# Optimization experiments

Measured on AMD Instinct MI355X. Metric: run time of the kernel, lower is better.

Reference implementation:

```python
import jax, jax.numpy as jnp
import numpy as np

B, S, H, NH = 2, 2048, 1024, 16
DH = H // NH
FF = 4 * H
EPS = 1e-5


def setup_inputs() -> dict:
    key = jax.random.key(0)
    ks = jax.random.split(key, 16)
    sd = 0.02
    inp = {
        "x": jax.random.normal(ks[0], (B, S, H), dtype=jnp.float32),
        "Wq": jax.random.normal(ks[1], (H, H), dtype=jnp.float32) * sd,
        "bq": jnp.zeros((H,), jnp.float32),
        "Wk": jax.random.normal(ks[2], (H, H), dtype=jnp.float32) * sd,
        "bk": jnp.zeros((H,), jnp.float32),
        "Wv": jax.random.normal(ks[3], (H, H), dtype=jnp.float32) * sd,
        "bv": jnp.zeros((H,), jnp.float32),
        "Wo": jax.random.normal(ks[4], (H, H), dtype=jnp.float32) * sd,
        "bo": jnp.zeros((H,), jnp.float32),
        "W1": jax.random.normal(ks[5], (H, FF), dtype=jnp.float32) * sd,
        "b1": jnp.zeros((FF,), jnp.float32),
        "W2": jax.random.normal(ks[6], (FF, H), dtype=jnp.float32) * sd,
        "b2": jnp.zeros((H,), jnp.float32),
        "g1": jnp.ones((H,), jnp.float32),
        "be1": jnp.zeros((H,), jnp.float32),
        "g2": jnp.ones((H,), jnp.float32),
        "be2": jnp.zeros((H,), jnp.float32),
    }
    return inp


def _layernorm(x, g, b):
    mu = jnp.mean(x, axis=-1, keepdims=True)
    var = jnp.mean(jnp.square(x - mu), axis=-1, keepdims=True)
    return (x - mu) * jax.lax.rsqrt(var + EPS) * g + b


def _block(x, Wq, bq, Wk, bk, Wv, bv, Wo, bo, W1, b1, W2, b2, g1, be1, g2, be2):
    # pre-LN attention
    h = _layernorm(x, g1, be1)
    q = (h @ Wq + bq).reshape(B, S, NH, DH)
    k = (h @ Wk + bk).reshape(B, S, NH, DH)
    v = (h @ Wv + bv).reshape(B, S, NH, DH)
    scale = DH ** -0.5
    scores = jnp.einsum("bqhd,bkhd->bhqk", q, k) * scale  # [B,NH,S,S]
    causal = jnp.tril(jnp.ones((S, S), dtype=bool))
    scores = jnp.where(causal, scores, -jnp.inf)
    attn = jax.nn.softmax(scores, axis=-1)
    out = jnp.einsum("bhqk,bkhd->bqhd", attn, v).reshape(B, S, H)
    x = x + (out @ Wo + bo)
    # pre-LN FFN with exact GELU (torch nn.GELU default)
    h = _layernorm(x, g2, be2)
    h = jax.nn.gelu(h @ W1 + b1, approximate=False)
    return x + (h @ W2 + b2)


def reference(x, Wq, bq, Wk, bk, Wv, bv, Wo, bo, W1, b1, W2, b2, g1, be1, g2, be2):
    return _block(x, Wq, bq, Wk, bk, Wv, bv, Wo, bo, W1, b1, W2, b2, g1, be1, g2, be2)
```

## Files before the change

### kernel.cpp

```cpp
#include <hip/hip_runtime.h>
#include <cstdint>
#include <cstddef>

typedef unsigned short u16;
typedef __attribute__((ext_vector_type(8))) __bf16 bf16v8;
typedef __attribute__((ext_vector_type(8))) unsigned short u16x8;
typedef __attribute__((ext_vector_type(4))) float f32x4;

constexpr int Bc = 2, Sc = 2048, Hc = 1024, NHc = 16, DHc = 64, FFc = 4096;
constexpr int Mc = Bc * Sc;

__device__ __forceinline__ u16 f2bf(float f) {
  unsigned u = __builtin_bit_cast(unsigned, f);
  return (u16)((u + 0x7FFFu + ((u >> 16) & 1u)) >> 16);
}

__device__ __forceinline__ int xcd_swz(int bid, int n) {
  const int q = n >> 3;
  return (bid & 7) * q + (bid >> 3);
}

__device__ __forceinline__ void gload_lds16(const void* g, void* l) {
  __builtin_amdgcn_global_load_lds(
      (const __attribute__((address_space(1))) unsigned*)(uintptr_t)g,
      (__attribute__((address_space(3))) unsigned*)(unsigned)(uintptr_t)l,
      16, 0, 0);
}

__global__ __launch_bounds__(256) void wconv_kernel(const float* __restrict__ W,
                                                    u16* __restrict__ Wt, int K, int N) {
  __shared__ float tile[64][65];
  const int n0 = blockIdx.x << 6, k0 = blockIdx.y << 6;
  const int t = threadIdx.x;
  const int col = t & 63, r0 = t >> 6;
#pragma unroll
  for (int i = 0; i < 16; ++i) {
    int r = (i << 2) + r0;
    tile[r][col] = W[(size_t)(k0 + r) * N + n0 + col];
  }
  __syncthreads();
#pragma unroll
  for (int i = 0; i < 16; ++i) {
    int n = (i << 2) + r0;
    Wt[(size_t)(n0 + n) * K + k0 + col] = f2bf(tile[col][n]);
  }
}

__global__ __launch_bounds__(256) void ln_kernel(const float* __restrict__ x,
                                                 const float* __restrict__ g,
                                                 const float* __restrict__ be,
                                                 u16* __restrict__ y) {
  const int row = blockIdx.x;
  const int t = threadIdx.x;
  const float4 v = ((const float4*)(x + (size_t)row * Hc))[t];
  float s1 = v.x + v.y + v.z + v.w;
  float s2 = v.x * v.x + v.y * v.y + v.z * v.z + v.w * v.w;
#pragma unroll
  for (int o = 32; o > 0; o >>= 1) {
    s1 += __shfl_xor(s1, o);
    s2 += __shfl_xor(s2, o);
  }
  __shared__ float r1[4], r2[4];
  const int wave = t >> 6, lane = t & 63;
  if (lane == 0) { r1[wave] = s1; r2[wave] = s2; }
  __syncthreads();
  s1 = r1[0] + r1[1] + r1[2] + r1[3];
  s2 = r2[0] + r2[1] + r2[2] + r2[3];
  const float mu = s1 * (1.f / Hc);
  const float var = s2 * (1.f / Hc) - mu * mu;
  const float rs = rsqrtf(var + 1e-5f);
  const float4 gv = ((const float4*)g)[t];
  const float4 bv = ((const float4*)be)[t];
  ushort4 ov;
  ov.x = f2bf((v.x - mu) * rs * gv.x + bv.x);
  ov.y = f2bf((v.y - mu) * rs * gv.y + bv.y);
  ov.z = f2bf((v.z - mu) * rs * gv.z + bv.z);
  ov.w = f2bf((v.w - mu) * rs * gv.w + bv.w);
  ((ushort4*)(y + (size_t)row * Hc))[t] = ov;
}

template <int EPI>
__global__ __launch_bounds__(256, 2) void gemm_kernel(
    const u16* __restrict__ A, const u16* __restrict__ Bt,
    const float* __restrict__ bias, const float* __restrict__ res,
    u16* __restrict__ outb, float* __restrict__ outf, float* __restrict__ outf2,
    int N, int Kext, int lda, int ldb, int koff, int nx) {
  __shared__ __align__(16) char smraw[32768];
  u16 (*As)[128][32] = (u16(*)[128][32])smraw;
  u16 (*Bs)[128][32] = (u16(*)[128][32])(smraw + 16384);
  float (*Cs)[16][132] = (float(*)[16][132])smraw;

  const int t = threadIdx.x;
  const int wave = t >> 6, lane = t & 63;
  const int pid = xcd_swz(blockIdx.x, gridDim.x);
  const int bn = pid % nx, bm = pid / nx;
  const int kz = blockIdx.z;
  A += (size_t)kz * koff;
  Bt += (size_t)kz * koff;
  const int wm = wave >> 1, wn = wave & 1;
  const int fr = lane & 15, fk = (lane >> 4) << 3;

  f32x4 acc[4][4] = {};

  const int srow = (wave << 4) + (lane >> 2);
  const int scol = (lane & 3) << 3;
  const u16* Ag0 = A + (size_t)(bm * 128 + srow) * lda + scol;
  const u16* Ag1 = Ag0 + (size_t)64 * lda;
  const u16* Bg0 = Bt + (size_t)(bn * 128 + srow) * ldb + scol;
  const u16* Bg1 = Bg0 + (size_t)64 * ldb;

  const int nk = Kext >> 5;
  auto STAGE = [&](int buf, int k0) {
    gload_lds16(Ag0 + k0, &As[buf][wave << 4][0]);
    gload_lds16(Ag1 + k0, &As[buf][64 + (wave << 4)][0]);
    gload_lds16(Bg0 + k0, &Bs[buf][wave << 4][0]);
    gload_lds16(Bg1 + k0, &Bs[buf][64 + (wave << 4)][0]);
  };

  STAGE(0, 0);
  asm volatile("s_waitcnt vmcnt(0)" ::: "memory");
  __syncthreads();
  int cur = 0;
  for (int kt = 0; kt < nk; ++kt) {
    if (kt + 1 < nk) STAGE(cur ^ 1, (kt + 1) << 5);
    bf16v8 af[4], bfr[4];
#pragma unroll
    for (int i = 0; i < 4; ++i) af[i] = *(const bf16v8*)&As[cur][(wm << 6) + (i << 4) + fr][fk];
#pragma unroll
    for (int j = 0; j < 4; ++j) bfr[j] = *(const bf16v8*)&Bs[cur][(wn << 6) + (j << 4) + fr][fk];
    __builtin_amdgcn_s_setprio(1);
#pragma unroll
    for (int i = 0; i < 4; ++i)
#pragma unroll
      for (int j = 0; j < 4; ++j)
        acc[i][j] = __builtin_amdgcn_mfma_f32_16x16x32_bf16(af[i], bfr[j], acc[i][j], 0, 0, 0);
    __builtin_amdgcn_s_setprio(0);
    asm volatile("s_waitcnt vmcnt(0)" ::: "memory");
    __syncthreads();
    cur ^= 1;
  }

  const int cr = (lane >> 4) << 2, cc = lane & 15;
  const int b2 = t >> 7, u = t & 127, lr = u >> 3, c0 = (u & 7) << 4;
  float* fdst = (EPI == 3 && kz) ? outf2 : outf;

  for (int i = 0; i < 4; ++i) {
#pragma unroll
    for (int j = 0; j < 4; ++j) {
      int col = (wn << 6) + (j << 4) + cc;
      float bz = 0.f;
      if constexpr (EPI != 3) bz = bias[(bn << 7) + col];
#pragma unroll
      for (int r = 0; r < 4; ++r) Cs[wm][cr + r][col] = acc[i][j][r] + bz;
    }
    __syncthreads();
    {
      const float* crow = &Cs[b2][lr][c0];
      f32x4 v0 = *(const f32x4*)(crow);
      f32x4 v1 = *(const f32x4*)(crow + 4);
      f32x4 v2 = *(const f32x4*)(crow + 8);
      f32x4 v3 = *(const f32x4*)(crow + 12);
      const int grow = (bm << 7) + (b2 << 6) + (i << 4) + lr;
      const int gc = (bn << 7) + c0;
      const size_t base = (size_t)grow * N + gc;
      if constexpr (EPI == 0 || EPI == 1) {
        float vv[16];
#pragma unroll
        for (int k = 0; k < 4; ++k) { vv[k] = v0[k]; vv[4 + k] = v1[k]; vv[8 + k] = v2[k]; vv[12 + k] = v3[k]; }
        if constexpr (EPI == 1) {
#pragma unroll
          for (int k = 0; k < 16; ++k)
            vv[k] = 0.5f * vv[k] * (1.0f + erff(vv[k] * 0.70710678118654752f));
        }
        u16x8 o0, o1;
#pragma unroll
        for (int k = 0; k < 8; ++k) { o0[k] = f2bf(vv[k]); o1[k] = f2bf(vv[8 + k]); }
        *(u16x8*)&outb[base] = o0;
        *(u16x8*)&outb[base + 8] = o1;
      } else {
        if constexpr (EPI == 2) {
          const f32x4* rp = (const f32x4*)&res[base];
          v0 += rp[0]; v1 += rp[1]; v2 += rp[2]; v3 += rp[3];
        }
        f32x4* op = (f32x4*)&fdst[base];
        op[0] = v0; op[1] = v1; op[2] = v2; op[3] = v3;
      }
    }
    __syncthreads();
  }
}

__global__ __launch_bounds__(256, 2) void qkv_gemm_kernel(
    const u16* __restrict__ A, const u16* __restrict__ Bt,
    const float* __restrict__ bq, const float* __restrict__ bk,
    const float* __restrict__ bv,
    u16* __restrict__ Qb, u16* __restrict__ Kb, u16* __restrict__ Vtg) {
  constexpr int K = 1024;
  __shared__ __align__(16) char smraw[32768];
  u16 (*As)[128][32] = (u16(*)[128][32])smraw;
  u16 (*Bs)[128][32] = (u16(*)[128][32])(smraw + 16384);
  float (*Cs)[16][132] = (float(*)[16][132])smraw;

  const int t = threadIdx.x;
  const int wave = t >> 6, lane = t & 63;
  const int pid = xcd_swz(blockIdx.x, 768);
  const int bn = pid % 24, bm = pid / 24;
  const int wm = wave >> 1, wn = wave & 1;
  const int fr = lane & 15, fk = (lane >> 4) << 3;
  const int seg = bn >> 3;

  f32x4 acc[4][4] = {};

  const int srow = (wave << 4) + (lane >> 2);
  const int scol = (lane & 3) << 3;
  const u16* Ag0 = A + (size_t)(bm * 128 + srow) * K + scol;
  const u16* Ag1 = Ag0 + (size_t)64 * K;
  const u16* Bg0 = Bt + (size_t)(bn * 128 + srow) * K + scol;
  const u16* Bg1 = Bg0 + (size_t)64 * K;

  const int nk = K >> 5;
  auto STAGE = [&](int buf, int k0) {
    gload_lds16(Ag0 + k0, &As[buf][wave << 4][0]);
    gload_lds16(Ag1 + k0, &As[buf][64 + (wave << 4)][0]);
    gload_lds16(Bg0 + k0, &Bs[buf][wave << 4][0]);
    gload_lds16(Bg1 + k0, &Bs[buf][64 + (wave << 4)][0]);
  };

  STAGE(0, 0);
  asm volatile("s_waitcnt vmcnt(0)" ::: "memory");
  __syncthreads();
  int cur = 0;
  for (int kt = 0; kt < nk; ++kt) {
    if (kt + 1 < nk) STAGE(cur ^ 1, (kt + 1) << 5);
    bf16v8 af[4], bfr[4];
#pragma unroll
    for (int i = 0; i < 4; ++i) af[i] = *(const bf16v8*)&As[cur][(wm << 6) + (i << 4) + fr][fk];
#pragma unroll
    for (int j = 0; j < 4; ++j) bfr[j] = *(const bf16v8*)&Bs[cur][(wn << 6) + (j << 4) + fr][fk];
    __builtin_amdgcn_s_setprio(1);
#pragma unroll
    for (int i = 0; i < 4; ++i)
#pragma unroll
      for (int j = 0; j < 4; ++j)
        acc[i][j] = __builtin_amdgcn_mfma_f32_16x16x32_bf16(af[i], bfr[j], acc[i][j], 0, 0, 0);
    __builtin_amdgcn_s_setprio(0);
    asm volatile("s_waitcnt vmcnt(0)" ::: "memory");
    __syncthreads();
    cur ^= 1;
  }

  const int cr = (lane >> 4) << 2, cc = lane & 15;
  const int b2 = t >> 7, u = t & 127, lr = u >> 3, c0 = (u & 7) << 4;
  const float* bp = (seg == 0) ? bq : (seg == 1) ? bk : bv;

  for (int i = 0; i < 4; ++i) {
#pragma unroll
    for (int j = 0; j < 4; ++j) {
      int col = (wn << 6) + (j << 4) + cc;
      float bz = bp[((bn << 7) + col) & 1023];
#pragma unroll
      for (int r = 0; r < 4; ++r) Cs[wm][cr + r][col] = acc[i][j][r] + bz;
    }
    __syncthreads();
    if (seg < 2) {
      const float* crow = &Cs[b2][lr][c0];
      f32x4 v0 = *(const f32x4*)(crow);
      f32x4 v1 = *(const f32x4*)(crow + 4);
      f32x4 v2 = *(const f32x4*)(crow + 8);
      f32x4 v3 = *(const f32x4*)(crow + 12);
      const int grow = (bm << 7) + (b2 << 6) + (i << 4) + lr;
      const int cn0 = (((bn & 7) << 7) + c0);
      u16* dst = (seg == 0) ? Qb : Kb;
      u16x8 o0, o1;
#pragma unroll
      for (int k = 0; k < 4; ++k) {
        o0[k] = f2bf(v0[k]); o0[4 + k] = f2bf(v1[k]);
        o1[k] = f2bf(v2[k]); o1[4 + k] = f2bf(v3[k]);
      }
      *(u16x8*)&dst[(size_t)grow * 1024 + cn0] = o0;
      *(u16x8*)&dst[(size_t)grow * 1024 + cn0 + 8] = o1;
    } else {
      const int cv = ((bn & 7) << 7) + u;
      const int h = cv >> 6, dh = cv & 63;
#pragma unroll
      for (int oct = 0; oct < 2; ++oct) {
        u16x8 o;
#pragma unroll
        for (int k = 0; k < 8; ++k) o[k] = f2bf(Cs[b2][(oct << 3) + k][u]);
        const int srow2 = (bm << 7) + (b2 << 6) + (i << 4) + (oct << 3);
        const int bb = srow2 >> 11, s = srow2 & 2047;
        size_t idx = ((size_t)(bb * 16 + h)) * (64 * 2048) + (size_t)dh * 2048 + s;
        *(u16x8*)&Vtg[idx] = o;
      }
    }
    __syncthreads();
  }
}

__global__ __launch_bounds__(256) void combine_kernel(float* __restrict__ out,
                                                      const float* __restrict__ p0,
                                                      const float* __restrict__ p1,
                                                      const float* __restrict__ bias) {
  const int i = blockIdx.x * 256 + threadIdx.x;
  f32x4 o = ((f32x4*)out)[i];
  f32x4 a = ((const f32x4*)p0)[i];
  f32x4 b = ((const f32x4*)p1)[i];
  const int col = (i << 2) & 1023;
  f32x4 bb = *(const f32x4*)&bias[col];
  o += a + b + bb;
  ((f32x4*)out)[i] = o;
}

__global__ __launch_bounds__(256, 3) void attn_kernel(const u16* __restrict__ Q,
                                                      const u16* __restrict__ Kb,
                                                      const u16* __restrict__ Vt,
                                                      u16* __restrict__ O) {
  constexpr float CS = 0.18033688011112042f;
  constexpr float M2 = 8.0f;
  const int pid = xcd_swz(blockIdx.x, 512);
  const int bx = pid & 15, bh = pid >> 4;
  const int t = threadIdx.x, wave = t >> 6, lane = t & 63;
  const int fr = lane & 15, fk = (lane >> 4) << 3;

  __shared__ u16 Ks[2][64][72];
  __shared__ u16 Vs[2][64][72];
  __shared__ u16 Ps[4][16][72];

  const size_t base = ((size_t)(bh >> 4) * Sc) * Hc + (bh & 15) * DHc;
  const u16* Qp = Q + base;
  const u16* Kp = Kb + base;
  const u16* Vp = Vt + (size_t)bh * (64 * 2048);

  const int r_st = t >> 3;
  const int co_st = (t & 7) << 3;

  bf16v8 ones;
#pragma unroll
  for (int k = 0; k < 8; ++k) ones[k] = (__bf16)1.0f;

  for (int half = 0; half < 2; ++half) {
    const int qt = half ? (31 - bx) : bx;
    const int q0 = qt << 6;
    const int nt = qt + 1;

    const int qrow = q0 + (wave << 4) + fr;
    const bf16v8 qf0 = *(const bf16v8*)&Qp[(size_t)qrow * Hc + fk];
    const bf16v8 qf1 = *(const bf16v8*)&Qp[(size_t)qrow * Hc + 32 + fk];

    f32x4 oacc[4] = {};
    f32x4 osum = {};

    const int crow0 = q0 + (wave << 4) + ((lane >> 4) << 2);

    u16x8 rk0, rk1, rv0, rv1;
    auto LD = [&](int kv0) {
      rk0 = *(const u16x8*)&Kp[(size_t)(kv0 + r_st) * Hc + co_st];
      rk1 = *(const u16x8*)&Kp[(size_t)(kv0 + 32 + r_st) * Hc + co_st];
      rv0 = *(const u16x8*)&Vp[(size_t)r_st * 2048 + kv0 + co_st];
      rv1 = *(const u16x8*)&Vp[(size_t)(32 + r_st) * 2048 + kv0 + co_st];
    };
    auto WR = [&](int buf) {
      *(u16x8*)&Ks[buf][r_st][co_st] = rk0;
      *(u16x8*)&Ks[buf][32 + r_st][co_st] = rk1;
      *(u16x8*)&Vs[buf][r_st][co_st] = rv0;
      *(u16x8*)&Vs[buf][32 + r_st][co_st] = rv1;
    };

    LD(0);
    WR(0);
    __syncthreads();
    int cur = 0;
    for (int it = 0; it < nt; ++it) {
      const int kv0 = it << 6;
      const bool hasnext = (it + 1 < nt);
      if (hasnext) LD(kv0 + 64);

      f32x4 sc[4];
      __builtin_amdgcn_s_setprio(1);
#pragma unroll
      for (int c = 0; c < 4; ++c) {
        bf16v8 kf0 = *(const bf16v8*)&Ks[cur][(c << 4) + fr][fk];
        bf16v8 kf1 = *(const bf16v8*)&Ks[cur][(c << 4) + fr][32 + fk];
        f32x4 a = {0.f, 0.f, 0.f, 0.f};
        a = __builtin_amdgcn_mfma_f32_16x16x32_bf16(qf0, kf0, a, 0, 0, 0);
        a = __builtin_amdgcn_mfma_f32_16x16x32_bf16(qf1, kf1, a, 0, 0, 0);
        sc[c] = a;
      }
      __builtin_amdgcn_s_setprio(0);

      if (kv0 + 64 > q0) {
#pragma unroll
        for (int c = 0; c < 4; ++c)
#pragma unroll
          for (int r = 0; r < 4; ++r) {
            int kv = kv0 + (c << 4) + fr;
            if (kv > crow0 + r) sc[c][r] = -INFINITY;
          }
      }

#pragma unroll
      for (int c = 0; c < 4; ++c)
#pragma unroll
        for (int r = 0; r < 4; ++r) {
          float p = exp2f(fmaf(sc[c][r], CS, -M2));
          Ps[wave][((lane >> 4) << 2) + r][(c << 4) + fr] = f2bf(p);
        }

      const bf16v8 pa0 = *(const bf16v8*)&Ps[wave][fr][fk];
      const bf16v8 pa1 = *(const bf16v8*)&Ps[wave][fr][32 + fk];
      __builtin_amdgcn_s_setprio(1);
#pragma unroll
      for (int f = 0; f < 4; ++f) {
        bf16v8 vf0 = *(const bf16v8*)&Vs[cur][(f << 4) + fr][fk];
        bf16v8 vf1 = *(const bf16v8*)&Vs[cur][(f << 4) + fr][32 + fk];
        oacc[f] = __builtin_amdgcn_mfma_f32_16x16x32_bf16(pa0, vf0, oacc[f], 0, 0, 0);
        oacc[f] = __builtin_amdgcn_mfma_f32_16x16x32_bf16(pa1, vf1, oacc[f], 0, 0, 0);
      }
      osum = __builtin_amdgcn_mfma_f32_16x16x32_bf16(pa0, ones, osum, 0, 0, 0);
      osum = __builtin_amdgcn_mfma_f32_16x16x32_bf16(pa1, ones, osum, 0, 0, 0);
      __builtin_amdgcn_s_setprio(0);

      if (hasnext) WR(cur ^ 1);
      __syncthreads();
      cur ^= 1;
    }
#pragma unroll
    for (int r = 0; r < 4; ++r) {
      float inv = 1.0f / osum[r];
      int row = crow0 + r;
#pragma unroll
      for (int f = 0; f < 4; ++f)
        O[base + (size_t)row * Hc + (f << 4) + fr] = f2bf(oacc[f][r] * inv);
    }
    __syncthreads();
  }
}

extern "C" void kernel_launch(void* const* d_in, const int* in_sizes, int n_in,
                              void* d_out, int out_size, void* d_ws, size_t ws_size,
                              hipStream_t stream) {
  const float* x  = (const float*)d_in[0];
  const float* Wq = (const float*)d_in[1];
  const float* bq = (const float*)d_in[2];
  const float* Wk = (const float*)d_in[3];
  const float* bk = (const float*)d_in[4];
  const float* Wv = (const float*)d_in[5];
  const float* bv = (const float*)d_in[6];
  const float* Wo = (const float*)d_in[7];
  const float* bo = (const float*)d_in[8];
  const float* W1 = (const float*)d_in[9];
  const float* b1 = (const float*)d_in[10];
  const float* W2 = (const float*)d_in[11];
  const float* b2 = (const float*)d_in[12];
  const float* g1 = (const float*)d_in[13];
  const float* be1 = (const float*)d_in[14];
  const float* g2 = (const float*)d_in[15];
  const float* be2 = (const float*)d_in[16];
  float* out = (float*)d_out;

  char* ws = (char*)d_ws;
  const size_t MB = 1024 * 1024;
  u16* wqkv = (u16*)(ws + 0 * MB);
  u16* wo   = (u16*)(ws + 6 * MB);
  u16* w1   = (u16*)(ws + 8 * MB);
  u16* w2   = (u16*)(ws + 16 * MB);
  u16* lnb  = (u16*)(ws + 24 * MB);
  u16* Qb   = (u16*)(ws + 32 * MB);
  u16* Kb   = (u16*)(ws + 40 * MB);
  u16* Vtg  = (u16*)(ws + 48 * MB);
  u16* Ob   = (u16*)(ws + 56 * MB);
  u16* H1   = (u16*)(ws + 32 * MB);
  float* p0 = (float*)(ws + 64 * MB);
  float* p1 = (float*)(ws + 0 * MB);

  dim3 blk(256);
  wconv_kernel<<<dim3(16, 16), blk, 0, stream>>>(Wq, wqkv, 1024, 1024);
  wconv_kernel<<<dim3(16, 16), blk, 0, stream>>>(Wk, wqkv + (size_t)1024 * 1024, 1024, 1024);
  wconv_kernel<<<dim3(16, 16), blk, 0, stream>>>(Wv, wqkv + (size_t)2048 * 1024, 1024, 1024);
  wconv_kernel<<<dim3(16, 16), blk, 0, stream>>>(Wo, wo, 1024, 1024);
  wconv_kernel<<<dim3(64, 16), blk, 0, stream>>>(W1, w1, 1024, 4096);
  wconv_kernel<<<dim3(16, 64), blk, 0, stream>>>(W2, w2, 4096, 1024);

  ln_kernel<<<Mc, blk, 0, stream>>>(x, g1, be1, lnb);

  qkv_gemm_kernel<<<dim3(768), blk, 0, stream>>>(lnb, wqkv, bq, bk, bv, Qb, Kb, Vtg);

  attn_kernel<<<dim3(512), blk, 0, stream>>>(Qb, Kb, Vtg, Ob);

  gemm_kernel<2><<<dim3(256), blk, 0, stream>>>(Ob, wo, bo, x, nullptr, out, nullptr,
                                                1024, 1024, 1024, 1024, 0, 8);

  ln_kernel<<<Mc, blk, 0, stream>>>(out, g2, be2, lnb);

  gemm_kernel<1><<<dim3(1024), blk, 0, stream>>>(lnb, w1, b1, nullptr, H1, nullptr, nullptr,
                                                 4096, 1024, 1024, 1024, 0, 32);

  gemm_kernel<3><<<dim3(256, 1, 2), blk, 0, stream>>>(H1, w2, nullptr, nullptr, nullptr, p0, p1,
                                                      1024, 2048, 4096, 4096, 2048, 8);
  combine_kernel<<<dim3(4096), blk, 0, stream>>>(out, p0, p1, b2);
}
```

Before: 260.2 us.

## Use 256x256 tiled GEMM for FFN up-projection and batch QKVO weight conversion

Adds a 512-thread GEMM kernel with 256x256 output tiles and 64-wide K steps, double-buffered in 128KB of LDS through direct global-to-LDS loads, and uses it for the W1 GEMM with a fused bias and exact-GELU epilogue. Larger tiles raise arithmetic intensity and cut redundant global reads of A and B. Separately, the four square weight conversions are merged into one launch to reduce launch overhead. The cost is much higher LDS and register use per block, so fewer blocks can be resident, and the grid shrinks to 256 blocks. The staging layout also has no swizzle, so LDS bank conflicts are possible.

```diff
diff --git a/kernel.cpp b/kernel.cpp
--- a/kernel.cpp
+++ b/kernel.cpp
@@ -25,6 +25,28 @@
       (const __attribute__((address_space(1))) unsigned*)(uintptr_t)g,
       (__attribute__((address_space(3))) unsigned*)(unsigned)(uintptr_t)l,
       16, 0, 0);
+}
+
+struct WP4 { const float* w0; const float* w1; const float* w2; const float* w3; };
+__global__ __launch_bounds__(256) void wconv4_kernel(WP4 p, u16* __restrict__ Wt) {
+  __shared__ float tile[64][65];
+  const float* W = (blockIdx.z == 0) ? p.w0 : (blockIdx.z == 1) ? p.w1
+                  : (blockIdx.z == 2) ? p.w2 : p.w3;
+  u16* dst = Wt + (size_t)blockIdx.z * 1024 * 1024;
+  const int n0 = blockIdx.x << 6, k0 = blockIdx.y << 6;
+  const int t = threadIdx.x;
+  const int col = t & 63, r0 = t >> 6;
+#pragma unroll
+  for (int i = 0; i < 16; ++i) {
+    int r = (i << 2) + r0;
+    tile[r][col] = W[(size_t)(k0 + r) * 1024 + n0 + col];
+  }
+  __syncthreads();
+#pragma unroll
+  for (int i = 0; i < 16; ++i) {
+    int n = (i << 2) + r0;
+    dst[(size_t)(n0 + n) * 1024 + k0 + col] = f2bf(tile[col][n]);
+  }
 }
 
 __global__ __launch_bounds__(256) void wconv_kernel(const float* __restrict__ W,
@@ -77,6 +99,105 @@
   ov.z = f2bf((v.z - mu) * rs * gv.z + bv.z);
   ov.w = f2bf((v.w - mu) * rs * gv.w + bv.w);
   ((ushort4*)(y + (size_t)row * Hc))[t] = ov;
+}
+
+template <int EPI>
+__global__ __launch_bounds__(512, 2) void gemm256_kernel(
+    const u16* __restrict__ A, const u16* __restrict__ Bt,
+    const float* __restrict__ bias, u16* __restrict__ outb,
+    int N, int K, int lda, int ldb, int nx) {
+  __shared__ __align__(16) char smraw[131072];
+  u16 (*As)[256][64] = (u16(*)[256][64])smraw;
+  u16 (*Bs)[256][64] = (u16(*)[256][64])(smraw + 65536);
+  float (*Cs)[260] = (float(*)[260])smraw;
+
+  const int t = threadIdx.x;
+  const int w = t >> 6, l = t & 63;
+  const int pid = xcd_swz(blockIdx.x, gridDim.x);
+  const int bn = pid % nx, bm = pid / nx;
+  const int wr = w >> 2, wn = w & 3;
+  const int fr = l & 15, fk = (l >> 4) << 3;
+
+  f32x4 acc[8][4] = {};
+
+  const int srow = (w << 3) + (l >> 3);
+  const int scol = (l & 7) << 3;
+  const u16* Ag = A + (size_t)(bm * 256 + srow) * lda + scol;
+  const u16* Bg = Bt + (size_t)(bn * 256 + srow) * ldb + scol;
+
+  auto STAGE = [&](int buf, int k0) {
+#pragma unroll
+    for (int i = 0; i < 4; ++i)
+      gload_lds16(Ag + (size_t)(i << 6) * lda + k0,
+                  smraw + (buf << 15) + (i << 13) + (w << 10));
+#pragma unroll
+    for (int i = 0; i < 4; ++i)
+      gload_lds16(Bg + (size_t)(i << 6) * ldb + k0,
+                  smraw + 65536 + (buf << 15) + (i << 13) + (w << 10));
+  };
+
+  const int nk = K >> 6;
+  STAGE(0, 0);
+  asm volatile("s_waitcnt vmcnt(0)" ::: "memory");
+  __syncthreads();
+  int cur = 0;
+  for (int kt = 0; kt < nk; ++kt) {
+    if (kt + 1 < nk) STAGE(cur ^ 1, (kt + 1) << 6);
+    bf16v8 bfr[4][2];
+#pragma unroll
+    for (int nj = 0; nj < 4; ++nj)
+#pragma unroll
+      for (int kh = 0; kh < 2; ++kh)
+        bfr[nj][kh] = *(const bf16v8*)&Bs[cur][(wn << 6) + (nj << 4) + fr][(kh << 5) + fk];
+    __builtin_amdgcn_s_setprio(1);
+#pragma unroll
+    for (int mi = 0; mi < 8; ++mi) {
+      const bf16v8 a0 = *(const bf16v8*)&As[cur][(wr << 7) + (mi << 4) + fr][fk];
+      const bf16v8 a1 = *(const bf16v8*)&As[cur][(wr << 7) + (mi << 4) + fr][32 + fk];
+#pragma unroll
+      for (int nj = 0; nj < 4; ++nj) {
+        acc[mi][nj] = __builtin_amdgcn_mfma_f32_16x16x32_bf16(a0, bfr[nj][0], acc[mi][nj], 0, 0, 0);
+        acc[mi][nj] = __builtin_amdgcn_mfma_f32_16x16x32_bf16(a1, bfr[nj][1], acc[mi][nj], 0, 0, 0);
+      }
+    }
+    __builtin_amdgcn_s_setprio(0);
+    asm volatile("s_waitcnt vmcnt(0)" ::: "memory");
+    __syncthreads();
+    cur ^= 1;
+  }
+
+  const int cr = (l >> 4) << 2, cc = l & 15;
+  const int row32 = t >> 4, col16 = (t & 15) << 4;
+#pragma unroll
+  for (int mi = 0; mi < 8; ++mi) {
+#pragma unroll
+    for (int nj = 0; nj < 4; ++nj) {
+      const int col = (wn << 6) + (nj << 4) + cc;
+      const float bz = bias[(bn << 8) + col];
+#pragma unroll
+      for (int r = 0; r < 4; ++r) Cs[(wr << 4) + cr + r][col] = acc[mi][nj][r] + bz;
+    }
+    __syncthreads();
+    {
+      const float* crow = &Cs[row32][col16];
+      float vv[16];
+#pragma unroll
+      for (int k = 0; k < 16; ++k) vv[k] = crow[k];
+      if constexpr (EPI == 1) {
+#pragma unroll
+        for (int k = 0; k < 16; ++k)
+          vv[k] = 0.5f * vv[k] * (1.0f + erff(vv[k] * 0.70710678118654752f));
+      }
+      u16x8 o0, o1;
+#pragma unroll
+      for (int k = 0; k < 8; ++k) { o0[k] = f2bf(vv[k]); o1[k] = f2bf(vv[8 + k]); }
+      const int grow = (bm << 8) + ((row32 >> 4) << 7) + (mi << 4) + (row32 & 15);
+      const size_t base = (size_t)grow * N + (bn << 8) + col16;
+      *(u16x8*)&outb[base] = o0;
+      *(u16x8*)&outb[base + 8] = o1;
+    }
+    __syncthreads();
+  }
 }
 
 template <int EPI>
@@ -474,10 +595,8 @@
   float* p1 = (float*)(ws + 0 * MB);
 
   dim3 blk(256);
-  wconv_kernel<<<dim3(16, 16), blk, 0, stream>>>(Wq, wqkv, 1024, 1024);
-  wconv_kernel<<<dim3(16, 16), blk, 0, stream>>>(Wk, wqkv + (size_t)1024 * 1024, 1024, 1024);
-  wconv_kernel<<<dim3(16, 16), blk, 0, stream>>>(Wv, wqkv + (size_t)2048 * 1024, 1024, 1024);
-  wconv_kernel<<<dim3(16, 16), blk, 0, stream>>>(Wo, wo, 1024, 1024);
+  WP4 wp{Wq, Wk, Wv, Wo};
+  wconv4_kernel<<<dim3(16, 16, 4), blk, 0, stream>>>(wp, wqkv);
   wconv_kernel<<<dim3(64, 16), blk, 0, stream>>>(W1, w1, 1024, 4096);
   wconv_kernel<<<dim3(16, 64), blk, 0, stream>>>(W2, w2, 4096, 1024);
 
@@ -492,8 +611,8 @@
 
   ln_kernel<<<Mc, blk, 0, stream>>>(out, g2, be2, lnb);
 
-  gemm_kernel<1><<<dim3(1024), blk, 0, stream>>>(lnb, w1, b1, nullptr, H1, nullptr, nullptr,
-                                                 4096, 1024, 1024, 1024, 0, 32);
+  gemm256_kernel<1><<<dim3(256), dim3(512), 0, stream>>>(lnb, w1, b1, H1,
+                                                         4096, 1024, 1024, 1024, 16);
 
   gemm_kernel<3><<<dim3(256, 1, 2), blk, 0, stream>>>(H1, w2, nullptr, nullptr, nullptr, p0, p1,
                                                       1024, 2048, 4096, 4096, 2048, 8);
```

Measured after the change: 283.2 us. 1.09x slower.
